# Optimization experiments

Measured on AMD Instinct MI355X. Metric: run time of the kernel, lower is better.

## Reference

```python
import jax, jax.numpy as jnp
import numpy as np

N_ATOMS = 5000
N_PAIRS = 160000
N_STRUCT = 16
N_SPECIES = 4
L_MAX = 2
K = 128            # k_max per l (rectangular)
N_BASIS = 8        # radial basis size
RAD_HIDDEN = 32    # radial MLP hidden
CUTOFF = 5.0
MSG_SCALE = 0.1767767   # ~1/sqrt(avg_degree)
INIT_SCALE = 0.2        # hypers['initial_scaling']


def _orthogonal(key, n):
    m = jax.random.normal(key, (n, n))
    q, r = jnp.linalg.qr(m)
    return q * jnp.sign(jnp.diag(r))[None, :]


def setup_inputs() -> dict:
    key = jax.random.key(0)
    ks = jax.random.split(key, 24)
    positions = jax.random.normal(ks[0], (N_ATOMS, 3)) * 1.5
    cells = jax.random.normal(ks[1], (N_STRUCT, 3, 3)) * 0.5
    species = jax.random.randint(ks[2], (N_ATOMS,), 0, N_SPECIES)
    cell_shifts = jax.random.randint(ks[3], (N_PAIRS, 3), 0, 3).astype(jnp.int32)
    center_indices = jax.random.randint(ks[4], (N_PAIRS,), 0, N_ATOMS)
    neighbor_indices = jax.random.randint(ks[5], (N_PAIRS,), 0, N_ATOMS)
    structure_pairs = jax.random.randint(ks[6], (N_PAIRS,), 0, N_STRUCT)
    s = lambda k, sh, f: jax.random.normal(k, sh) * f
    params = dict(
        embed=s(ks[7], (N_SPECIES, K), 1.0),
        rad_w1=s(ks[8], (N_BASIS, RAD_HIDDEN), 0.3), rad_b1=jnp.zeros((RAD_HIDDEN,)),
        rad_w2=s(ks[9], (RAD_HIDDEN, (L_MAX + 1) * K), 0.3), rad_b2=jnp.zeros(((L_MAX + 1) * K,)),
        erad_w1=s(ks[10], (N_BASIS, RAD_HIDDEN), 0.3), erad_b1=jnp.zeros((RAD_HIDDEN,)),
        erad_w2=s(ks[11], (RAD_HIDDEN, (L_MAX + 1) * K), 0.3), erad_b2=jnp.zeros(((L_MAX + 1) * K,)),
        mix_a=s(ks[12], (L_MAX + 1, K), 0.5),
        emix_a=s(ks[13], (L_MAX + 1, K), 0.5),
        head_w1=s(ks[14], (K, K), 0.1), head_b1=jnp.zeros((K,)),
        head_w2=s(ks[15], (K, K), 0.1), head_b2=jnp.zeros((K,)),
        last_w=s(ks[16], (K, 1), 0.1), last_b=jnp.zeros((1,)),
        U2=_orthogonal(ks[20], 9),  # orthogonal CG change-of-basis, U @ U.T = I
    )
    return dict(positions=positions, cells=cells, species=species,
                cell_shifts=cell_shifts, center_indices=center_indices,
                neighbor_indices=neighbor_indices, structure_pairs=structure_pairs,
                **params)


def _sph(unit):
    # real spherical harmonics up to l=2, inputs are unit vectors [P,3]
    x, y, z = unit[:, 0], unit[:, 1], unit[:, 2]
    sh0 = jnp.ones_like(x)[:, None]
    sh1 = jnp.stack([y, z, x], axis=1)
    c = jnp.sqrt(3.0)
    sh2 = jnp.stack([c * x * y, c * y * z, 0.5 * (3 * z * z - 1.0),
                     c * x * z, 0.5 * c * (x * x - y * y)], axis=1)
    return [sh0, sh1, sh2]


def _radial(d, w1, b1, w2, b2):
    # Gaussian radial basis * smooth cutoff -> MLP -> per-l K channels
    centers = jnp.linspace(0.0, CUTOFF, N_BASIS)
    rb = jnp.exp(-((d[:, None] - centers[None, :]) ** 2) / (2.0 * 0.5 ** 2))
    fcut = jnp.where(d < CUTOFF, 0.5 * (jnp.cos(jnp.pi * d / CUTOFF) + 1.0), 0.0)
    h = jax.nn.silu((rb * fcut[:, None]) @ w1 + b1)
    return (h @ w2 + b2).reshape(-1, L_MAX + 1, K)  # [P, l, K]


def _uncouple(f, l, U2):
    # coupled [N, 2l+1, K] -> uncoupled matrix [N, 3, 3, K] (padded_l = 2)
    if l == 0:
        return f[:, :, None, :]
    n, _, k = f.shape
    vec = jnp.zeros((n, 9, k), f.dtype)
    off = 1 if l == 1 else 4
    vec = vec.at[:, off:off + 2 * l + 1, :].set(f)
    unc = jnp.einsum('qp,nqk->npk', U2, vec)  # U2.T @ vec
    return unc.reshape(n, 3, 3, k)


def _couple(unc, l, U2):
    if l == 0:
        return unc[:, :, 0, :]
    n, k = unc.shape[0], unc.shape[-1]
    vec = jnp.einsum('pq,nqk->npk', U2, unc.reshape(n, 9, k))
    off = 1 if l == 1 else 4
    return vec[:, off:off + 2 * l + 1, :]


def _cg_iterate(feats, U2, mix):
    # CG tensor product iteration in the uncoupled (matrix) basis:
    # matrix product A@A is equivariant under A -> D A D^T
    out = []
    for l, f in enumerate(feats):
        A = _uncouple(f, l, U2)
        C = jnp.einsum('nimk,nmjk->nijk', A, A)
        out.append(_couple(A + C * mix[l][None, None, None, :], l, U2))
    return out


def _forward(positions, cells, embed, rad_w1, rad_b1, rad_w2, rad_b2,
             erad_w1, erad_b1, erad_w2, erad_b2, mix_a, emix_a,
             head_w1, head_b1, head_w2, head_b2, last_w, last_b, U2,
             species, cell_shifts, center_indices, neighbor_indices, structure_pairs):
    # pair vectors with PBC shifts
    shifts = cell_shifts.astype(positions.dtype) - 1.0  # -> {-1,0,1}
    vec = positions[neighbor_indices] - positions[center_indices] \
        + jnp.einsum('pi,pij->pj', shifts, cells[structure_pairs])
    d = jnp.sqrt(jnp.sum(vec * vec, axis=1) + 1e-12)
    unit = vec / d[:, None]
    sh = [s * INIT_SCALE for s in _sph(unit)]
    Rk = _radial(d, rad_w1, rad_b1, rad_w2, rad_b2)      # [P, 3, K]
    emb_n = embed[species][neighbor_indices]             # [P, K]

    # invariant message passing: sh_l x radial x neighbor embedding, scatter to centers
    feats = []
    for l in range(L_MAX + 1):
        msg = sh[l][:, :, None] * Rk[:, l, None, :] * emb_n[:, None, :]
        feats.append(jax.ops.segment_sum(msg, center_indices, num_segments=N_ATOMS) * MSG_SCALE)

    feats = _cg_iterate(feats, U2, mix_a)

    # equivariant message passing layer
    Rke = _radial(d, erad_w1, erad_b1, erad_w2, erad_b2)
    inv_n = feats[0][neighbor_indices, 0, :]             # [P, K] invariant part
    new = []
    for l in range(L_MAX + 1):
        g = feats[l][neighbor_indices]                   # [P, 2l+1, K]
        msg = sh[l][:, :, None] * Rke[:, l, None, :] * inv_n[:, None, :] \
            + Rke[:, 0, None, :] * g
        new.append(feats[l] + jax.ops.segment_sum(msg, center_indices, num_segments=N_ATOMS) * MSG_SCALE)

    feats = _cg_iterate(new, U2, emix_a)

    # scalar (l=0) MLP head + last linear layer
    h = feats[0][:, 0, :]
    h = jax.nn.silu(h @ head_w1 + head_b1)
    h = jax.nn.silu(h @ head_w2 + head_b2)
    return h @ last_w + last_b  # [N_ATOMS, 1]


def reference(positions, cells, species, cell_shifts, center_indices,
              neighbor_indices, structure_pairs, embed, rad_w1, rad_b1, rad_w2,
              rad_b2, erad_w1, erad_b1, erad_w2, erad_b2, mix_a, emix_a,
              head_w1, head_b1, head_w2, head_b2, last_w, last_b, U2):
    return _forward(positions, cells, embed, rad_w1, rad_b1, rad_w2, rad_b2,
                    erad_w1, erad_b1, erad_w2, erad_b2, mix_a, emix_a,
                    head_w1, head_b1, head_w2, head_b2, last_w, last_b, U2,
                    species, cell_shifts, center_indices, neighbor_indices,
                    structure_pairs)
```

## Files before the change

kernel.cpp:

```cpp
#include <hip/hip_runtime.h>

constexpr int   kAtoms  = 5000;
constexpr int   kPairs  = 160000;
constexpr int   KD      = 128;
constexpr int   NB      = 8;
constexpr int   RH      = 32;
constexpr float kCutoff = 5.0f;
constexpr float kPi     = 3.14159265358979323846f;
constexpr float C1 = 0.2f * 0.1767767f;
constexpr float C2 = 1.2f * 0.1767767f;

__device__ __forceinline__ float silu(float x) { return x / (1.0f + __expf(-x)); }
__device__ __forceinline__ void wave_fence() { __builtin_amdgcn_wave_barrier(); }


__global__ __launch_bounds__(256) void hist_kernel(
    const int* __restrict__ ctr, int* __restrict__ cnt)
{
    int p = blockIdx.x * 256 + threadIdx.x;
    atomicAdd(cnt + ctr[p], 1);
}

__global__ __launch_bounds__(1024) void scan_kernel(
    const int* __restrict__ cnt, int* __restrict__ off, int* __restrict__ cur)
{
    __shared__ int s_part[1024];
    const int CH = 5;
    int t = threadIdx.x;
    int base = t * CH;
    int loc[CH];
    int run = 0;
    #pragma unroll
    for (int i = 0; i < CH; i++) {
        int idx = base + i;
        int v = (idx < kAtoms) ? cnt[idx] : 0;
        loc[i] = run;
        run += v;
    }
    s_part[t] = run;
    __syncthreads();
    for (int st = 1; st < 1024; st <<= 1) {
        int v = (t >= st) ? s_part[t - st] : 0;
        __syncthreads();
        s_part[t] += v;
        __syncthreads();
    }
    int excl = (t > 0) ? s_part[t - 1] : 0;
    #pragma unroll
    for (int i = 0; i < CH; i++) {
        int idx = base + i;
        if (idx < kAtoms) { off[idx] = excl + loc[i]; cur[idx] = excl + loc[i]; }
    }
    if (t == 1023) off[kAtoms] = s_part[1023];
}

__global__ __launch_bounds__(256) void build_kernel(
    const float* __restrict__ pos, const float* __restrict__ cells,
    const int* __restrict__ species, const int* __restrict__ shifts,
    const int* __restrict__ ctr, const int* __restrict__ nbr,
    const int* __restrict__ spair,
    const float* __restrict__ ew1, const float* __restrict__ eb1,
    int* __restrict__ cur, int* __restrict__ nbrs_s, int* __restrict__ specs_s,
    float* __restrict__ rbf_s, float* __restrict__ hbuf)
{
    int p = blockIdx.x * 256 + threadIdx.x;
    int ci = ctr[p], ni = nbr[p], sp = spair[p];
    float s0 = (float)shifts[p * 3 + 0] - 1.0f;
    float s1 = (float)shifts[p * 3 + 1] - 1.0f;
    float s2 = (float)shifts[p * 3 + 2] - 1.0f;
    const float* C = cells + sp * 9;
    float vx = pos[ni * 3 + 0] - pos[ci * 3 + 0] + s0 * C[0] + s1 * C[3] + s2 * C[6];
    float vy = pos[ni * 3 + 1] - pos[ci * 3 + 1] + s0 * C[1] + s1 * C[4] + s2 * C[7];
    float vz = pos[ni * 3 + 2] - pos[ci * 3 + 2] + s0 * C[2] + s1 * C[5] + s2 * C[8];
    float d = sqrtf(vx * vx + vy * vy + vz * vz + 1e-12f);
    float fcut = (d < kCutoff) ? 0.5f * (__cosf(kPi * d / kCutoff) + 1.0f) : 0.0f;

    int slot = atomicAdd(cur + ci, 1);
    nbrs_s[slot]  = ni;
    specs_s[slot] = species[ni];

    float r[NB];
    #pragma unroll
    for (int i = 0; i < NB; i++) {
        float tt = d - (kCutoff / (NB - 1)) * (float)i;
        r[i] = __expf(-2.0f * tt * tt) * fcut;
    }
    float4* rdst = (float4*)(rbf_s + (size_t)slot * NB);
    rdst[0] = make_float4(r[0], r[1], r[2], r[3]);
    rdst[1] = make_float4(r[4], r[5], r[6], r[7]);

    float* hdst = hbuf + (size_t)slot * RH;
    #pragma unroll
    for (int jq = 0; jq < RH / 4; jq++) {
        float4 hv; float* pv = (float*)&hv;
        #pragma unroll
        for (int u = 0; u < 4; u++) {
            int j = 4 * jq + u;
            float acc = eb1[j];
            #pragma unroll
            for (int i = 0; i < NB; i++) acc += r[i] * ew1[i * RH + j];
            pv[u] = silu(acc);
        }
        *(float4*)(hdst + 4 * jq) = hv;
    }
}

__global__ __launch_bounds__(256) void f0_kernel(
    const float* __restrict__ rbf_s, const int* __restrict__ specs_s,
    const int* __restrict__ off,
    const float* __restrict__ embed,
    const float* __restrict__ w1, const float* __restrict__ b1,
    const float* __restrict__ w2, const float* __restrict__ b2,
    const float* __restrict__ mix,
    float* __restrict__ G0)
{
    __shared__ float s_w1[NB][RH];
    __shared__ float s_b1v[RH];
    __shared__ float s_H[4][2][4][RH];
    __shared__ float s_Hc[4][4][RH];
    __shared__ float s_n[4][2][4];

    int t = threadIdx.x, w = t >> 6, lane = t & 63;
    for (int idx = t; idx < NB * RH; idx += 256)
        s_w1[idx >> 5][idx & 31] = w1[idx];
    if (t < RH) s_b1v[t] = b1[t];
    __syncthreads();

    int a = blockIdx.x * 4 + w;
    int start = off[a], m = off[a + 1] - start;

    int g = lane >> 5, j = lane & 31;
    float H0 = 0, H1 = 0, H2 = 0, H3 = 0;
    int   n0 = 0, n1 = 0, n2 = 0, n3 = 0;
    float b1j = s_b1v[j];
    for (int pr = g; pr < m; pr += 2) {
        const float* rb = rbf_s + (size_t)(start + pr) * NB;
        float acc = b1j;
        #pragma unroll
        for (int i = 0; i < NB; i++) acc += rb[i] * s_w1[i][j];
        float h = silu(acc);
        int s = specs_s[start + pr];
        H0 += (s == 0) ? h : 0.0f;  H1 += (s == 1) ? h : 0.0f;
        H2 += (s == 2) ? h : 0.0f;  H3 += (s == 3) ? h : 0.0f;
        n0 += (s == 0); n1 += (s == 1); n2 += (s == 2); n3 += (s == 3);
    }
    s_H[w][g][0][j] = H0; s_H[w][g][1][j] = H1;
    s_H[w][g][2][j] = H2; s_H[w][g][3][j] = H3;
    if (j == 0) {
        s_n[w][g][0] = (float)n0; s_n[w][g][1] = (float)n1;
        s_n[w][g][2] = (float)n2; s_n[w][g][3] = (float)n3;
    }
    wave_fence();
    #pragma unroll
    for (int e = lane; e < 4 * RH; e += 64) {
        int s = e >> 5, jj = e & 31;
        s_Hc[w][s][jj] = s_H[w][0][s][jj] + s_H[w][1][s][jj];
    }
    wave_fence();
    float nc0 = s_n[w][0][0] + s_n[w][1][0];
    float nc1 = s_n[w][0][1] + s_n[w][1][1];
    float nc2 = s_n[w][0][2] + s_n[w][1][2];
    float nc3 = s_n[w][0][3] + s_n[w][1][3];

    #pragma unroll
    for (int half = 0; half < 2; half++) {
        int k = lane + 64 * half;
        float e0 = embed[0 * KD + k], e1 = embed[1 * KD + k];
        float e2 = embed[2 * KD + k], e3 = embed[3 * KD + k];
        float P0 = 0, P1 = 0, P2 = 0, P3 = 0;
        #pragma unroll
        for (int jq = 0; jq < RH / 4; jq++) {
            float4 h0 = *(const float4*)&s_Hc[w][0][4 * jq];
            float4 h1 = *(const float4*)&s_Hc[w][1][4 * jq];
            float4 h2 = *(const float4*)&s_Hc[w][2][4 * jq];
            float4 h3 = *(const float4*)&s_Hc[w][3][4 * jq];
            float wa = w2[(4 * jq + 0) * (3 * KD) + k];
            float wb = w2[(4 * jq + 1) * (3 * KD) + k];
            float wc = w2[(4 * jq + 2) * (3 * KD) + k];
            float wd = w2[(4 * jq + 3) * (3 * KD) + k];
            P0 += h0.x * wa + h0.y * wb + h0.z * wc + h0.w * wd;
            P1 += h1.x * wa + h1.y * wb + h1.z * wc + h1.w * wd;
            P2 += h2.x * wa + h2.y * wb + h2.z * wc + h2.w * wd;
            P3 += h3.x * wa + h3.y * wb + h3.z * wc + h3.w * wd;
        }
        float F = b2[k] * (nc0 * e0 + nc1 * e1 + nc2 * e2 + nc3 * e3)
                + e0 * P0 + e1 * P1 + e2 * P2 + e3 * P3;
        float F0v = C1 * F;
        G0[(size_t)a * KD + k] = F0v + F0v * F0v * mix[k];
    }
}

__global__ void d0head_kernel(
    const float* __restrict__ hbuf, const int* __restrict__ nbrs_s,
    const int* __restrict__ off,
    const float* __restrict__ w2, const float* __restrict__ b2,
    const float* __restrict__ emix,
    const float* __restrict__ G0,
    const float* __restrict__ hw1, const float* __restrict__ hb1,
    const float* __restrict__ hw2, const float* __restrict__ hb2,
    const float* __restrict__ lw, const float* __restrict__ lb,
    float* __restrict__ out)
{
    __shared__ float s_v[4][KD];
    __shared__ float s_m[4][KD];

    int t = threadIdx.x, w = t >> 6, lane = t & 63;
    int a = blockIdx.x * 4 + w;
    int start = __builtin_amdgcn_readfirstlane(off[a]);
    int end   = __builtin_amdgcn_readfirstlane(off[a + 1]);

    int k0 = 2 * lane, k1 = 2 * lane + 1;
    float w2c0[RH], w2c1[RH];
    #pragma unroll
    for (int j = 0; j < RH; j++) {
        float2 wv = *(const float2*)&w2[j * (3 * KD) + k0];
        w2c0[j] = wv.x; w2c1[j] = wv.y;
    }
    float b2k0 = b2[k0], b2k1 = b2[k1];

    float D0 = 0.0f, D1 = 0.0f;
    for (int i = start; i < end; i++) {
        int nb = __builtin_amdgcn_readfirstlane(nbrs_s[i]);
        const float* h = hbuf + (size_t)i * RH;
        float2 gv = *(const float2*)(G0 + (size_t)nb * KD + k0);
        float4 h4[RH / 4];
        #pragma unroll
        for (int q = 0; q < RH / 4; q++) h4[q] = *(const float4*)(h + 4 * q);
        float R0 = b2k0, R1 = b2k1;
        #pragma unroll
        for (int q = 0; q < RH / 4; q++) {
            R0 += h4[q].x * w2c0[4*q+0] + h4[q].y * w2c0[4*q+1]
                + h4[q].z * w2c0[4*q+2] + h4[q].w * w2c0[4*q+3];
            R1 += h4[q].x * w2c1[4*q+0] + h4[q].y * w2c1[4*q+1]
                + h4[q].z * w2c1[4*q+2] + h4[q].w * w2c1[4*q+3];
        }
        D0 += R0 * gv.x;
        D1 += R1 * gv.y;
    }
    {
        float2 ga = *(const float2*)(G0 + (size_t)a * KD + k0);
        float q0 = ga.x + C2 * D0, q1 = ga.y + C2 * D1;
        s_v[w][k0] = q0 + q0 * q0 * emix[k0];
        s_v[w][k1] = q1 + q1 * q1 * emix[k1];
    }
    __syncthreads();

    int j = t & 127, grp = t >> 7;
    int a0 = grp * 2, a1 = grp * 2 + 1;
    float acc0 = hb1[j], acc1 = acc0;
    for (int kk = 0; kk < KD; kk += 4) {
        float wa = hw1[(kk+0)*KD+j], wb = hw1[(kk+1)*KD+j];
        float wc = hw1[(kk+2)*KD+j], wd = hw1[(kk+3)*KD+j];
        float4 v0 = *(const float4*)&s_v[a0][kk];
        float4 v1 = *(const float4*)&s_v[a1][kk];
        acc0 += v0.x*wa + v0.y*wb + v0.z*wc + v0.w*wd;
        acc1 += v1.x*wa + v1.y*wb + v1.z*wc + v1.w*wd;
    }
    s_m[a0][j] = silu(acc0);
    s_m[a1][j] = silu(acc1);
    __syncthreads();
    acc0 = hb2[j]; acc1 = acc0;
    for (int kk = 0; kk < KD; kk += 4) {
        float wa = hw2[(kk+0)*KD+j], wb = hw2[(kk+1)*KD+j];
        float wc = hw2[(kk+2)*KD+j], wd = hw2[(kk+3)*KD+j];
        float4 v0 = *(const float4*)&s_m[a0][kk];
        float4 v1 = *(const float4*)&s_m[a1][kk];
        acc0 += v0.x*wa + v0.y*wb + v0.z*wc + v0.w*wd;
        acc1 += v1.x*wa + v1.y*wb + v1.z*wc + v1.w*wd;
    }
    float lwj = lw[j];
    __syncthreads();
    s_v[a0][j] = silu(acc0) * lwj;
    s_v[a1][j] = silu(acc1) * lwj;
    __syncthreads();
    for (int s = 64; s > 0; s >>= 1) {
        if (j < s) {
            s_v[a0][j] += s_v[a0][j + s];
            s_v[a1][j] += s_v[a1][j + s];
        }
        __syncthreads();
    }
    if (t < 4) out[blockIdx.x * 4 + t] = s_v[t][0] + lb[0];
}

extern "C" void kernel_launch(void* const* d_in, const int* in_sizes, int n_in,
                              void* d_out, int out_size, void* d_ws, size_t ws_size,
                              hipStream_t stream) {
    const float* positions = (const float*)d_in[0];
    const float* cells     = (const float*)d_in[1];
    const int*   species   = (const int*)d_in[2];
    const int*   shifts    = (const int*)d_in[3];
    const int*   ctr       = (const int*)d_in[4];
    const int*   nbr       = (const int*)d_in[5];
    const int*   spair     = (const int*)d_in[6];
    const float* embed     = (const float*)d_in[7];
    const float* rad_w1    = (const float*)d_in[8];
    const float* rad_b1    = (const float*)d_in[9];
    const float* rad_w2    = (const float*)d_in[10];
    const float* rad_b2    = (const float*)d_in[11];
    const float* erad_w1   = (const float*)d_in[12];
    const float* erad_b1   = (const float*)d_in[13];
    const float* erad_w2   = (const float*)d_in[14];
    const float* erad_b2   = (const float*)d_in[15];
    const float* mix_a     = (const float*)d_in[16];
    const float* emix_a    = (const float*)d_in[17];
    const float* head_w1   = (const float*)d_in[18];
    const float* head_b1   = (const float*)d_in[19];
    const float* head_w2   = (const float*)d_in[20];
    const float* head_b2   = (const float*)d_in[21];
    const float* last_w    = (const float*)d_in[22];
    const float* last_b    = (const float*)d_in[23];

    float* rbf_s = (float*)d_ws;
    float* hbuf  = rbf_s + (size_t)kPairs * NB;
    float* G0    = hbuf + (size_t)kPairs * RH;
    int*   cnt   = (int*)(G0 + (size_t)kAtoms * KD);
    int*   off   = cnt + kAtoms;
    int*   cur   = off + kAtoms + 1;
    int*   nbrs  = cur + kAtoms;
    int*   specs = nbrs + kPairs;

    hipMemsetAsync(cnt, 0, kAtoms * sizeof(int), stream);

    hist_kernel<<<kPairs / 256, 256, 0, stream>>>(ctr, cnt);
    scan_kernel<<<1, 1024, 0, stream>>>(cnt, off, cur);
    build_kernel<<<kPairs / 256, 256, 0, stream>>>(
        positions, cells, species, shifts, ctr, nbr, spair,
        erad_w1, erad_b1, cur, nbrs, specs, rbf_s, hbuf);

    f0_kernel<<<kAtoms / 4, 256, 0, stream>>>(
        rbf_s, specs, off, embed, rad_w1, rad_b1, rad_w2, rad_b2,
        mix_a, G0);

    d0head_kernel<<<kAtoms / 4, 256, 0, stream>>>(
        hbuf, nbrs, off, erad_w2, erad_b2, emix_a, G0,
        head_w1, head_b1, head_w2, head_b2, last_w, last_b,
        (float*)d_out);
}
```

Measured before the change: 233.0 us.

## Fuse histogram and scan into one block; stage per-atom pair chunks in LDS

The separate histogram and scan kernels and the memset become a single one-block kernel that counts centers with LDS atomics before scanning. The f0 and d0head kernels now load 32-pair chunks of radial features, species and neighbor indices cooperatively into shared memory, then loop over them. The f0 kernel also replaces its LDS half-wave reduction with cross-lane shuffles. This cuts launch overhead and makes the per-pair global reads coalesced, but one block now serially processes 160k atomics, and the chunked loops read slightly past each atom's segment end.

```diff
diff --git a/kernel.cpp b/kernel.cpp
--- a/kernel.cpp
+++ b/kernel.cpp
@@ -14,36 +14,30 @@
 __device__ __forceinline__ void wave_fence() { __builtin_amdgcn_wave_barrier(); }
 
 
-__global__ __launch_bounds__(256) void hist_kernel(
-    const int* __restrict__ ctr, int* __restrict__ cnt)
+__global__ __launch_bounds__(1024) void csr_kernel(
+    const int* __restrict__ ctr, int* __restrict__ off, int* __restrict__ cur)
 {
-    int p = blockIdx.x * 256 + threadIdx.x;
-    atomicAdd(cnt + ctr[p], 1);
-}
-
-__global__ __launch_bounds__(1024) void scan_kernel(
-    const int* __restrict__ cnt, int* __restrict__ off, int* __restrict__ cur)
-{
+    __shared__ int lcnt[kAtoms];
     __shared__ int s_part[1024];
+    int t = threadIdx.x;
+    for (int i = t; i < kAtoms; i += 1024) lcnt[i] = 0;
+    __syncthreads();
+    for (int p = t; p < kPairs; p += 1024) atomicAdd(&lcnt[ctr[p]], 1);
+    __syncthreads();
+
     const int CH = 5;
-    int t = threadIdx.x;
-    int base = t * CH;
-    int loc[CH];
-    int run = 0;
+    int base = t * CH, loc[CH], run = 0;
     #pragma unroll
     for (int i = 0; i < CH; i++) {
         int idx = base + i;
-        int v = (idx < kAtoms) ? cnt[idx] : 0;
-        loc[i] = run;
-        run += v;
+        int v = (idx < kAtoms) ? lcnt[idx] : 0;
+        loc[i] = run; run += v;
     }
     s_part[t] = run;
     __syncthreads();
     for (int st = 1; st < 1024; st <<= 1) {
         int v = (t >= st) ? s_part[t - st] : 0;
-        __syncthreads();
-        s_part[t] += v;
-        __syncthreads();
+        __syncthreads(); s_part[t] += v; __syncthreads();
     }
     int excl = (t > 0) ? s_part[t - 1] : 0;
     #pragma unroll
@@ -61,7 +55,7 @@
     const int* __restrict__ spair,
     const float* __restrict__ ew1, const float* __restrict__ eb1,
     int* __restrict__ cur, int* __restrict__ nbrs_s, int* __restrict__ specs_s,
-    float* __restrict__ rbf_s, float* __restrict__ hbuf)
+    float* __restrict__ rbf_s, float* __restrict__ h2buf)
 {
     int p = blockIdx.x * 256 + threadIdx.x;
     int ci = ctr[p], ni = nbr[p], sp = spair[p];
@@ -89,7 +83,7 @@
     rdst[0] = make_float4(r[0], r[1], r[2], r[3]);
     rdst[1] = make_float4(r[4], r[5], r[6], r[7]);
 
-    float* hdst = hbuf + (size_t)slot * RH;
+    float* hdst = h2buf + (size_t)slot * RH;
     #pragma unroll
     for (int jq = 0; jq < RH / 4; jq++) {
         float4 hv; float* pv = (float*)&hv;
@@ -116,9 +110,9 @@
 {
     __shared__ float s_w1[NB][RH];
     __shared__ float s_b1v[RH];
-    __shared__ float s_H[4][2][4][RH];
-    __shared__ float s_Hc[4][4][RH];
-    __shared__ float s_n[4][2][4];
+    __shared__ float s_rb[4][32][NB];
+    __shared__ int   s_sp[4][32];
+    __shared__ float s_H[4][4][RH];
 
     int t = threadIdx.x, w = t >> 6, lane = t & 63;
     for (int idx = t; idx < NB * RH; idx += 256)
@@ -127,40 +121,42 @@
     __syncthreads();
 
     int a = blockIdx.x * 4 + w;
-    int start = off[a], m = off[a + 1] - start;
+    int start = off[a], end = off[a + 1];
 
     int g = lane >> 5, j = lane & 31;
+    float b1j = s_b1v[j];
     float H0 = 0, H1 = 0, H2 = 0, H3 = 0;
     int   n0 = 0, n1 = 0, n2 = 0, n3 = 0;
-    float b1j = s_b1v[j];
-    for (int pr = g; pr < m; pr += 2) {
-        const float* rb = rbf_s + (size_t)(start + pr) * NB;
-        float acc = b1j;
-        #pragma unroll
-        for (int i = 0; i < NB; i++) acc += rb[i] * s_w1[i][j];
-        float h = silu(acc);
-        int s = specs_s[start + pr];
-        H0 += (s == 0) ? h : 0.0f;  H1 += (s == 1) ? h : 0.0f;
-        H2 += (s == 2) ? h : 0.0f;  H3 += (s == 3) ? h : 0.0f;
-        n0 += (s == 0); n1 += (s == 1); n2 += (s == 2); n3 += (s == 3);
-    }
-    s_H[w][g][0][j] = H0; s_H[w][g][1][j] = H1;
-    s_H[w][g][2][j] = H2; s_H[w][g][3][j] = H3;
-    if (j == 0) {
-        s_n[w][g][0] = (float)n0; s_n[w][g][1] = (float)n1;
-        s_n[w][g][2] = (float)n2; s_n[w][g][3] = (float)n3;
+
+    for (int c = start; c < end; c += 32) {
+        int mm = min(32, end - c);
+        float4 rv = *((const float4*)(rbf_s + (size_t)c * NB) + lane);
+        ((float4*)s_rb[w])[lane] = rv;
+        if (lane < mm) s_sp[w][lane] = specs_s[c + lane];
+        wave_fence();
+        for (int pr = g; pr < mm; pr += 2) {
+            const float* rb = s_rb[w][pr];
+            float acc = b1j;
+            #pragma unroll
+            for (int i = 0; i < NB; i++) acc += rb[i] * s_w1[i][j];
+            float h = silu(acc);
+            int s = s_sp[w][pr];
+            H0 += (s == 0) ? h : 0.0f;  H1 += (s == 1) ? h : 0.0f;
+            H2 += (s == 2) ? h : 0.0f;  H3 += (s == 3) ? h : 0.0f;
+            n0 += (s == 0); n1 += (s == 1); n2 += (s == 2); n3 += (s == 3);
+        }
+        wave_fence();
+    }
+    H0 += __shfl_xor(H0, 32); H1 += __shfl_xor(H1, 32);
+    H2 += __shfl_xor(H2, 32); H3 += __shfl_xor(H3, 32);
+    n0 += __shfl_xor(n0, 32); n1 += __shfl_xor(n1, 32);
+    n2 += __shfl_xor(n2, 32); n3 += __shfl_xor(n3, 32);
+    if (lane < 32) {
+        s_H[w][0][j] = H0; s_H[w][1][j] = H1;
+        s_H[w][2][j] = H2; s_H[w][3][j] = H3;
     }
     wave_fence();
-    #pragma unroll
-    for (int e = lane; e < 4 * RH; e += 64) {
-        int s = e >> 5, jj = e & 31;
-        s_Hc[w][s][jj] = s_H[w][0][s][jj] + s_H[w][1][s][jj];
-    }
-    wave_fence();
-    float nc0 = s_n[w][0][0] + s_n[w][1][0];
-    float nc1 = s_n[w][0][1] + s_n[w][1][1];
-    float nc2 = s_n[w][0][2] + s_n[w][1][2];
-    float nc3 = s_n[w][0][3] + s_n[w][1][3];
+    float fn0 = (float)n0, fn1 = (float)n1, fn2 = (float)n2, fn3 = (float)n3;
 
     #pragma unroll
     for (int half = 0; half < 2; half++) {
@@ -170,10 +166,10 @@
         float P0 = 0, P1 = 0, P2 = 0, P3 = 0;
         #pragma unroll
         for (int jq = 0; jq < RH / 4; jq++) {
-            float4 h0 = *(const float4*)&s_Hc[w][0][4 * jq];
-            float4 h1 = *(const float4*)&s_Hc[w][1][4 * jq];
-            float4 h2 = *(const float4*)&s_Hc[w][2][4 * jq];
-            float4 h3 = *(const float4*)&s_Hc[w][3][4 * jq];
+            float4 h0 = *(const float4*)&s_H[w][0][4 * jq];
+            float4 h1 = *(const float4*)&s_H[w][1][4 * jq];
+            float4 h2 = *(const float4*)&s_H[w][2][4 * jq];
+            float4 h3 = *(const float4*)&s_H[w][3][4 * jq];
             float wa = w2[(4 * jq + 0) * (3 * KD) + k];
             float wb = w2[(4 * jq + 1) * (3 * KD) + k];
             float wc = w2[(4 * jq + 2) * (3 * KD) + k];
@@ -183,15 +179,15 @@
             P2 += h2.x * wa + h2.y * wb + h2.z * wc + h2.w * wd;
             P3 += h3.x * wa + h3.y * wb + h3.z * wc + h3.w * wd;
         }
-        float F = b2[k] * (nc0 * e0 + nc1 * e1 + nc2 * e2 + nc3 * e3)
+        float F = b2[k] * (fn0 * e0 + fn1 * e1 + fn2 * e2 + fn3 * e3)
                 + e0 * P0 + e1 * P1 + e2 * P2 + e3 * P3;
         float F0v = C1 * F;
         G0[(size_t)a * KD + k] = F0v + F0v * F0v * mix[k];
     }
 }
 
-__global__ void d0head_kernel(
-    const float* __restrict__ hbuf, const int* __restrict__ nbrs_s,
+__global__ __launch_bounds__(256) void d0head_kernel(
+    const float* __restrict__ h2buf, const int* __restrict__ nbrs_s,
     const int* __restrict__ off,
     const float* __restrict__ w2, const float* __restrict__ b2,
     const float* __restrict__ emix,
@@ -201,13 +197,14 @@
     const float* __restrict__ lw, const float* __restrict__ lb,
     float* __restrict__ out)
 {
+    __shared__ float s_h[4][32][RH];
+    __shared__ int   s_nbr[4][32];
     __shared__ float s_v[4][KD];
     __shared__ float s_m[4][KD];
 
     int t = threadIdx.x, w = t >> 6, lane = t & 63;
     int a = blockIdx.x * 4 + w;
-    int start = __builtin_amdgcn_readfirstlane(off[a]);
-    int end   = __builtin_amdgcn_readfirstlane(off[a + 1]);
+    int start = off[a], end = off[a + 1];
 
     int k0 = 2 * lane, k1 = 2 * lane + 1;
     float w2c0[RH], w2c1[RH];
@@ -219,23 +216,31 @@
     float b2k0 = b2[k0], b2k1 = b2[k1];
 
     float D0 = 0.0f, D1 = 0.0f;
-    for (int i = start; i < end; i++) {
-        int nb = __builtin_amdgcn_readfirstlane(nbrs_s[i]);
-        const float* h = hbuf + (size_t)i * RH;
-        float2 gv = *(const float2*)(G0 + (size_t)nb * KD + k0);
-        float4 h4[RH / 4];
+    for (int c = start; c < end; c += 32) {
+        int mm = min(32, end - c);
+        const float4* src = (const float4*)(h2buf + (size_t)c * RH);
         #pragma unroll
-        for (int q = 0; q < RH / 4; q++) h4[q] = *(const float4*)(h + 4 * q);
-        float R0 = b2k0, R1 = b2k1;
-        #pragma unroll
-        for (int q = 0; q < RH / 4; q++) {
-            R0 += h4[q].x * w2c0[4*q+0] + h4[q].y * w2c0[4*q+1]
-                + h4[q].z * w2c0[4*q+2] + h4[q].w * w2c0[4*q+3];
-            R1 += h4[q].x * w2c1[4*q+0] + h4[q].y * w2c1[4*q+1]
-                + h4[q].z * w2c1[4*q+2] + h4[q].w * w2c1[4*q+3];
-        }
-        D0 += R0 * gv.x;
-        D1 += R1 * gv.y;
+        for (int q = 0; q < 4; q++)
+            ((float4*)s_h[w])[q * 64 + lane] = src[q * 64 + lane];
+        if (lane < mm) s_nbr[w][lane] = nbrs_s[c + lane];
+        wave_fence();
+        #pragma unroll 2
+        for (int i = 0; i < mm; i++) {
+            int nb = s_nbr[w][i];
+            float2 gv = *(const float2*)(G0 + (size_t)nb * KD + k0);
+            float R0 = b2k0, R1 = b2k1;
+            #pragma unroll
+            for (int q = 0; q < RH / 4; q++) {
+                float4 h4 = *(const float4*)&s_h[w][i][4 * q];
+                R0 += h4.x * w2c0[4*q+0] + h4.y * w2c0[4*q+1]
+                    + h4.z * w2c0[4*q+2] + h4.w * w2c0[4*q+3];
+                R1 += h4.x * w2c1[4*q+0] + h4.y * w2c1[4*q+1]
+                    + h4.z * w2c1[4*q+2] + h4.w * w2c1[4*q+3];
+            }
+            D0 += R0 * gv.x;
+            D1 += R1 * gv.y;
+        }
+        wave_fence();
     }
     {
         float2 ga = *(const float2*)(G0 + (size_t)a * KD + k0);
@@ -312,28 +317,25 @@
     const float* last_b    = (const float*)d_in[23];
 
     float* rbf_s = (float*)d_ws;
-    float* hbuf  = rbf_s + (size_t)kPairs * NB;
-    float* G0    = hbuf + (size_t)kPairs * RH;
-    int*   cnt   = (int*)(G0 + (size_t)kAtoms * KD);
-    int*   off   = cnt + kAtoms;
+    float* h2buf = rbf_s + (size_t)kPairs * NB;
+    float* G0    = h2buf + (size_t)kPairs * RH;
+    int*   off   = (int*)(G0 + (size_t)kAtoms * KD);
     int*   cur   = off + kAtoms + 1;
     int*   nbrs  = cur + kAtoms;
     int*   specs = nbrs + kPairs;
 
-    hipMemsetAsync(cnt, 0, kAtoms * sizeof(int), stream);
-
-    hist_kernel<<<kPairs / 256, 256, 0, stream>>>(ctr, cnt);
-    scan_kernel<<<1, 1024, 0, stream>>>(cnt, off, cur);
+    csr_kernel<<<1, 1024, 0, stream>>>(ctr, off, cur);
+
     build_kernel<<<kPairs / 256, 256, 0, stream>>>(
         positions, cells, species, shifts, ctr, nbr, spair,
-        erad_w1, erad_b1, cur, nbrs, specs, rbf_s, hbuf);
+        erad_w1, erad_b1, cur, nbrs, specs, rbf_s, h2buf);
 
     f0_kernel<<<kAtoms / 4, 256, 0, stream>>>(
         rbf_s, specs, off, embed, rad_w1, rad_b1, rad_w2, rad_b2,
         mix_a, G0);
 
     d0head_kernel<<<kAtoms / 4, 256, 0, stream>>>(
-        hbuf, nbrs, off, erad_w2, erad_b2, emix_a, G0,
+        h2buf, nbrs, off, erad_w2, erad_b2, emix_a, G0,
         head_w1, head_b1, head_w2, head_b2, last_w, last_b,
         (float*)d_out);
 }
```

Result: no change. 233.3 us (+0.1%).
